# Kernel optimization log

Hardware: AMD Instinct MI355X
Metric: run time of the kernel (lower is better)

Reference implementation:

```python
import jax, jax.numpy as jnp
import numpy as np

B, T, D, H, C = 64, 1024, 128, 512, 2


def setup_inputs() -> dict:
    key = jax.random.key(0)
    ks = jax.random.split(key, 6)
    x = jax.random.normal(ks[0], (B, T, D), dtype=jnp.float32)
    labels = jax.random.randint(ks[1], (B, T), 0, C, dtype=jnp.int32)
    # Keras LSTMCell params: kernel [D,4H], recurrent_kernel [H,4H], bias [4H]
    Wx = jax.random.normal(ks[2], (D, 4 * H), dtype=jnp.float32) * (1.0 / np.sqrt(D))
    Wh = jax.random.normal(ks[3], (H, 4 * H), dtype=jnp.float32) * (1.0 / np.sqrt(H))
    b = jnp.zeros((4 * H,), dtype=jnp.float32).at[H:2 * H].set(1.0)  # unit forget bias
    Wo = jax.random.normal(ks[4], (H, C), dtype=jnp.float32) * (1.0 / np.sqrt(H))
    bo = jnp.zeros((C,), dtype=jnp.float32)
    return {"x": x, "labels": labels, "Wx": Wx, "Wh": Wh, "b": b, "Wo": Wo, "bo": bo}


def _lstm_logits(x, Wx, Wh, b, Wo, bo):
    # Precompute input contribution for all steps: [B,T,4H]
    xz = jnp.einsum('btd,dk->btk', x, Wx) + b

    def step(carry, z_t):
        h, c = carry
        z = z_t + h @ Wh                     # [B,4H]
        i, f, g, o = jnp.split(z, 4, axis=-1)  # keras gate order: i,f,c,o
        i = jax.nn.sigmoid(i)
        f = jax.nn.sigmoid(f)
        g = jnp.tanh(g)
        o = jax.nn.sigmoid(o)
        c = f * c + i * g
        h = o * jnp.tanh(c)
        return (h, c), h

    h0 = jnp.zeros((x.shape[0], Wh.shape[0]), dtype=x.dtype)
    (_, _), hs = jax.lax.scan(step, (h0, h0), jnp.swapaxes(xz, 0, 1))
    hs = jnp.swapaxes(hs, 0, 1)              # [B,T,H]
    return jnp.einsum('bth,hc->btc', hs, Wo) + bo  # [B,T,C]


def reference(x, labels, Wx, Wh, b, Wo, bo):
    logits = _lstm_logits(x, Wx, Wh, b, Wo, bo)
    logp = jax.nn.log_softmax(logits, axis=-1)
    prediction = jnp.exp(logp)               # softmax probs
    nll = -jnp.take_along_axis(logp, labels[..., None].astype(jnp.int32), axis=-1)[..., 0]
    cost = jnp.mean(nll)
    return prediction, cost
```

## Files before the change

kernel.cpp:

```cpp
#include <hip/hip_runtime.h>
#include <stdint.h>

#define TLEN 1024
#define BATCH 64
#define DIMX 128
#define HID 512

typedef __attribute__((ext_vector_type(8))) short short8;
typedef __attribute__((ext_vector_type(4))) float f32x4;
typedef __attribute__((ext_vector_type(4))) unsigned u32x4;

#define OFF_WT   0u
#define OFF_XBF  2621440u
#define OFF_HB   19398656u
#define OFF_ACC  19660800u
#define ZERO_LEN (262144u + 64u)

__device__ __forceinline__ unsigned short f2bf(float f) {
  unsigned u = __float_as_uint(f);
  u += 0x7fffu + ((u >> 16) & 1u);
  return (unsigned short)(u >> 16);
}
__device__ __forceinline__ float sigm(float x) { return 1.0f / (1.0f + __expf(-x)); }
__device__ __forceinline__ float tanh_fast(float x) {
  float a = fabsf(x);
  float e = __expf(2.0f * a);
  float t = 1.0f - 2.0f / (e + 1.0f);
  return copysignf(t, x);
}

__global__ void k_convx(const float4* __restrict__ x4, ushort4* __restrict__ o4) {
  int i = blockIdx.x * 256 + threadIdx.x;
  float4 v = x4[i];
  ushort4 o;
  o.x = f2bf(v.x); o.y = f2bf(v.y); o.z = f2bf(v.z); o.w = f2bf(v.w);
  o4[i] = o;
}

__global__ void k_tw(const float* __restrict__ Wx, const float* __restrict__ Wh,
                     unsigned short* __restrict__ Wt) {
  __shared__ float tile[32][65];
  int bk = blockIdx.x;
  int k0 = (bk / 64) * 64;
  int c0 = (bk % 64) * 32;
  int tid = threadIdx.x;
  const float* src = (k0 < 128) ? (Wx + (size_t)k0 * 2048)
                                : (Wh + (size_t)(k0 - 128) * 2048);
#pragma unroll
  for (int p = 0; p < 8; ++p) {
    int i = p * 256 + tid;
    int kk = i >> 5, cc = i & 31;
    tile[cc][kk] = src[(size_t)kk * 2048 + (c0 + cc)];
  }
  __syncthreads();
  int cc = tid >> 3, ch = tid & 7;
  unsigned short tmp[8];
#pragma unroll
  for (int j = 0; j < 8; ++j) tmp[j] = f2bf(tile[cc][ch * 8 + j]);
  uint4 o;
  o.x = (unsigned)tmp[0] | ((unsigned)tmp[1] << 16);
  o.y = (unsigned)tmp[2] | ((unsigned)tmp[3] << 16);
  o.z = (unsigned)tmp[4] | ((unsigned)tmp[5] << 16);
  o.w = (unsigned)tmp[6] | ((unsigned)tmp[7] << 16);
  *(uint4*)(Wt + (size_t)(c0 + cc) * 640 + k0 + ch * 8) = o;
}

__global__ __launch_bounds__(512, 1) void k_lstm(
    const unsigned short* __restrict__ xbf,
    const unsigned short* __restrict__ Wt,
    const float* __restrict__ bias,
    const float* __restrict__ Wo,
    unsigned* __restrict__ hb,
    float* __restrict__ out)
{
  __shared__ float red[2][4][4][8][32];
  __shared__ short8 xch[2][4][2][2][64];
  __shared__ unsigned xflag[2][4][2];

  const int tid  = threadIdx.x;
  const int w    = tid >> 6;
  const int kw   = w & 3;
  const int cg   = w >> 2;
  const int lane = tid & 63;
  const int q    = lane >> 4;
  const int m    = lane & 15;
  const int grp  = blockIdx.x & 7;
  const int hj   = blockIdx.x >> 3;
  const int g0   = grp * 8;

  if (tid < 16) xflag[tid >> 3][(tid >> 1) & 3][tid & 1] = 0;

  short8 Bf[5][4];
#pragma unroll
  for (int cc = 0; cc < 5; ++cc) {
#pragma unroll
    for (int j = 0; j < 4; ++j) {
      int gate = cg * 2 + (j >> 1);
      int col = gate * HID + hj * 32 + (j & 1) * 16 + m;
      int k = (cc == 0) ? (kw * 32 + q * 8)
                        : (128 + kw * 128 + (cc - 1) * 32 + q * 8);
      Bf[cc][j] = *(const short8*)(Wt + (size_t)col * 640 + k);
    }
  }

  const int col  = lane & 31;
  const int hcol = hj * 32 + col;
  float c_state = 0.0f;
  const float b_i = bias[0 * HID + hcol];
  const float b_f = bias[1 * HID + hcol];
  const float b_g = bias[2 * HID + hcol];
  const float b_o = bias[3 * HID + hcol];
  const float2 wo = ((const float2*)Wo)[hcol];

  const int ab = g0 + (m & 7);

  __syncthreads();

  short8 a0 = *(const short8*)(xbf + (size_t)ab * (TLEN * DIMX) + kw * 32 + q * 8);

#pragma unroll 1
  for (int t = 0; t < TLEN; ++t) {
    const unsigned* hin = hb + (size_t)(t & 1) * (BATCH * HID);
    const int buf = t & 1;

    const unsigned* pb = hin + (size_t)ab * HID + kw * 128 + cg * 64 + q * 8;
    u32x4 r0, r1, r2, r3;
    {
      const unsigned tg = (unsigned)t & 0xFFFFu;
      int guard = 0;
      for (;;) {
        asm volatile(
            "global_load_dwordx4 %0, %4, off sc0 sc1\n\t"
            "global_load_dwordx4 %1, %4, off offset:16 sc0 sc1\n\t"
            "global_load_dwordx4 %2, %4, off offset:128 sc0 sc1\n\t"
            "global_load_dwordx4 %3, %4, off offset:144 sc0 sc1\n\t"
            "s_waitcnt vmcnt(0)"
            : "=v"(r0), "=v"(r1), "=v"(r2), "=v"(r3)
            : "v"(pb)
            : "memory");
        unsigned d = (r0[0] ^ tg) | (r0[1] ^ tg) | (r0[2] ^ tg) | (r0[3] ^ tg);
        d |= (r1[0] ^ tg) | (r1[1] ^ tg) | (r1[2] ^ tg) | (r1[3] ^ tg);
        d |= (r2[0] ^ tg) | (r2[1] ^ tg) | (r2[2] ^ tg) | (r2[3] ^ tg);
        d |= (r3[0] ^ tg) | (r3[1] ^ tg) | (r3[2] ^ tg) | (r3[3] ^ tg);
        bool bad = (d & 0xFFFFu) != 0u;
        if (__ballot(bad) == 0ull || ++guard > (1 << 20)) break;
        __builtin_amdgcn_s_sleep(2);
      }
    }

    short8 f0, f1;
    {
      union { short8 s; unsigned u[4]; } pk;
      pk.u[0] = (r0[0] >> 16) | (r0[1] & 0xFFFF0000u);
      pk.u[1] = (r0[2] >> 16) | (r0[3] & 0xFFFF0000u);
      pk.u[2] = (r1[0] >> 16) | (r1[1] & 0xFFFF0000u);
      pk.u[3] = (r1[2] >> 16) | (r1[3] & 0xFFFF0000u);
      f0 = pk.s;
      pk.u[0] = (r2[0] >> 16) | (r2[1] & 0xFFFF0000u);
      pk.u[1] = (r2[2] >> 16) | (r2[3] & 0xFFFF0000u);
      pk.u[2] = (r3[0] >> 16) | (r3[1] & 0xFFFF0000u);
      pk.u[3] = (r3[2] >> 16) | (r3[3] & 0xFFFF0000u);
      f1 = pk.s;
    }

    xch[buf][kw][cg][0][lane] = f0;
    xch[buf][kw][cg][1][lane] = f1;
    __hip_atomic_store(&xflag[buf][kw][cg], (unsigned)(t + 1),
                       __ATOMIC_RELEASE, __HIP_MEMORY_SCOPE_WORKGROUP);
    {
      int guard = 0;
      while (__hip_atomic_load(&xflag[buf][kw][cg ^ 1], __ATOMIC_ACQUIRE,
                               __HIP_MEMORY_SCOPE_WORKGROUP) < (unsigned)(t + 1)) {
        if (++guard > (1 << 22)) break;
      }
    }
    short8 s0 = xch[buf][kw][cg ^ 1][0][lane];
    short8 s1 = xch[buf][kw][cg ^ 1][1][lane];

    short8 a1 = cg ? s0 : f0;
    short8 a2 = cg ? s1 : f1;
    short8 a3 = cg ? f0 : s0;
    short8 a4 = cg ? f1 : s1;

    f32x4 z0 = {0,0,0,0}, z1 = {0,0,0,0}, z2 = {0,0,0,0}, z3 = {0,0,0,0};
    z0 = __builtin_amdgcn_mfma_f32_16x16x32_bf16(a0, Bf[0][0], z0, 0, 0, 0);
    z1 = __builtin_amdgcn_mfma_f32_16x16x32_bf16(a0, Bf[0][1], z1, 0, 0, 0);
    z2 = __builtin_amdgcn_mfma_f32_16x16x32_bf16(a0, Bf[0][2], z2, 0, 0, 0);
    z3 = __builtin_amdgcn_mfma_f32_16x16x32_bf16(a0, Bf[0][3], z3, 0, 0, 0);
    z0 = __builtin_amdgcn_mfma_f32_16x16x32_bf16(a1, Bf[1][0], z0, 0, 0, 0);
    z1 = __builtin_amdgcn_mfma_f32_16x16x32_bf16(a1, Bf[1][1], z1, 0, 0, 0);
    z2 = __builtin_amdgcn_mfma_f32_16x16x32_bf16(a1, Bf[1][2], z2, 0, 0, 0);
    z3 = __builtin_amdgcn_mfma_f32_16x16x32_bf16(a1, Bf[1][3], z3, 0, 0, 0);
    z0 = __builtin_amdgcn_mfma_f32_16x16x32_bf16(a2, Bf[2][0], z0, 0, 0, 0);
    z1 = __builtin_amdgcn_mfma_f32_16x16x32_bf16(a2, Bf[2][1], z1, 0, 0, 0);
    z2 = __builtin_amdgcn_mfma_f32_16x16x32_bf16(a2, Bf[2][2], z2, 0, 0, 0);
    z3 = __builtin_amdgcn_mfma_f32_16x16x32_bf16(a2, Bf[2][3], z3, 0, 0, 0);
    z0 = __builtin_amdgcn_mfma_f32_16x16x32_bf16(a3, Bf[3][0], z0, 0, 0, 0);
    z1 = __builtin_amdgcn_mfma_f32_16x16x32_bf16(a3, Bf[3][1], z1, 0, 0, 0);
    z2 = __builtin_amdgcn_mfma_f32_16x16x32_bf16(a3, Bf[3][2], z2, 0, 0, 0);
    z3 = __builtin_amdgcn_mfma_f32_16x16x32_bf16(a3, Bf[3][3], z3, 0, 0, 0);
    z0 = __builtin_amdgcn_mfma_f32_16x16x32_bf16(a4, Bf[4][0], z0, 0, 0, 0);
    z1 = __builtin_amdgcn_mfma_f32_16x16x32_bf16(a4, Bf[4][1], z1, 0, 0, 0);
    z2 = __builtin_amdgcn_mfma_f32_16x16x32_bf16(a4, Bf[4][2], z2, 0, 0, 0);
    z3 = __builtin_amdgcn_mfma_f32_16x16x32_bf16(a4, Bf[4][3], z3, 0, 0, 0);

    {
      int tn = (t + 1 < TLEN) ? (t + 1) : t;
      a0 = *(const short8*)(xbf + ((size_t)ab * TLEN + tn) * DIMX +
                            kw * 32 + q * 8);
    }

    if (q < 2) {
#pragma unroll
      for (int r = 0; r < 4; ++r) {
        int rw = q * 4 + r;
        red[buf][kw][cg * 2 + 0][rw][0 * 16 + m] = z0[r];
        red[buf][kw][cg * 2 + 0][rw][1 * 16 + m] = z1[r];
        red[buf][kw][cg * 2 + 1][rw][0 * 16 + m] = z2[r];
        red[buf][kw][cg * 2 + 1][rw][1 * 16 + m] = z3[r];
      }
    }
    __syncthreads();

    if (lane < 32) {
      float zi = b_i + red[buf][0][0][w][col] + red[buf][1][0][w][col]
                     + red[buf][2][0][w][col] + red[buf][3][0][w][col];
      float zf = b_f + red[buf][0][1][w][col] + red[buf][1][1][w][col]
                     + red[buf][2][1][w][col] + red[buf][3][1][w][col];
      float zg = b_g + red[buf][0][2][w][col] + red[buf][1][2][w][col]
                     + red[buf][2][2][w][col] + red[buf][3][2][w][col];
      float zo = b_o + red[buf][0][3][w][col] + red[buf][1][3][w][col]
                     + red[buf][2][3][w][col] + red[buf][3][3][w][col];
      float ig = sigm(zi), fg = sigm(zf), gg = tanh_fast(zg), og = sigm(zo);
      c_state = fg * c_state + ig * gg;
      float hval = og * tanh_fast(c_state);

      unsigned hword = ((unsigned)f2bf(hval) << 16) | (unsigned)((t + 1) & 0xFFFF);
      int base = lane & ~3;
      unsigned w0 = __shfl(hword, base + 0);
      unsigned w1 = __shfl(hword, base + 1);
      unsigned w2 = __shfl(hword, base + 2);
      unsigned w3 = __shfl(hword, base + 3);
      if ((lane & 3) == 0) {
        u32x4 v4 = {w0, w1, w2, w3};
        unsigned* dst = hb + (size_t)((t + 1) & 1) * (BATCH * HID) +
                        (size_t)(g0 + w) * HID + hcol;
        asm volatile("global_store_dwordx4 %0, %1, off sc0 sc1"
                     :: "v"(dst), "v"(v4) : "memory");
      }

      float p0 = hval * wo.x, p1 = hval * wo.y;
      p0 += __shfl_xor(p0, 16); p1 += __shfl_xor(p1, 16);
      p0 += __shfl_xor(p0, 8);  p1 += __shfl_xor(p1, 8);
      p0 += __shfl_xor(p0, 4);  p1 += __shfl_xor(p1, 4);
      p0 += __shfl_xor(p0, 2);  p1 += __shfl_xor(p1, 2);
      p0 += __shfl_xor(p0, 1);  p1 += __shfl_xor(p1, 1);
      if (lane == 0) {
        float* po = out + ((size_t)(g0 + w) * TLEN + t) * 2;
        atomicAdd(po + 0, p0);
        atomicAdd(po + 1, p1);
      }
    }
  }
}

__global__ void k_out2(float* __restrict__ out, const float* __restrict__ bo,
                       const int* __restrict__ labels, float* __restrict__ acc) {
  __shared__ float sred[4];
  int i = blockIdx.x * 256 + threadIdx.x;
  float l0 = out[(size_t)i * 2 + 0] + bo[0];
  float l1 = out[(size_t)i * 2 + 1] + bo[1];
  float mx = fmaxf(l0, l1);
  float e0 = __expf(l0 - mx), e1 = __expf(l1 - mx);
  float s = e0 + e1, inv = 1.0f / s;
  out[(size_t)i * 2 + 0] = e0 * inv;
  out[(size_t)i * 2 + 1] = e1 * inv;
  int lab = labels[i];
  float nll = __logf(s) - ((lab ? l1 : l0) - mx);
#pragma unroll
  for (int off = 32; off >= 1; off >>= 1) nll += __shfl_xor(nll, off);
  if ((threadIdx.x & 63) == 0) sred[threadIdx.x >> 6] = nll;
  __syncthreads();
  if (threadIdx.x == 0)
    atomicAdd(acc, sred[0] + sred[1] + sred[2] + sred[3]);
}

__global__ void k_fin(const float* __restrict__ acc, float* __restrict__ out) {
  out[BATCH * TLEN * 2] = acc[0] * (1.0f / (float)(BATCH * TLEN));
}

extern "C" void kernel_launch(void* const* d_in, const int* in_sizes, int n_in,
                              void* d_out, int out_size, void* d_ws, size_t ws_size,
                              hipStream_t stream) {
  const float* x      = (const float*)d_in[0];
  const int*   labels = (const int*)d_in[1];
  const float* Wx     = (const float*)d_in[2];
  const float* Wh     = (const float*)d_in[3];
  const float* b      = (const float*)d_in[4];
  const float* Wo     = (const float*)d_in[5];
  const float* bo     = (const float*)d_in[6];
  float* out = (float*)d_out;
  char* ws = (char*)d_ws;

  unsigned short* Wt  = (unsigned short*)(ws + OFF_WT);
  unsigned short* xbf = (unsigned short*)(ws + OFF_XBF);
  unsigned*       hb  = (unsigned*)(ws + OFF_HB);
  float*          acc = (float*)(ws + OFF_ACC);

  hipMemsetAsync(ws + OFF_HB, 0, ZERO_LEN, stream);
  hipMemsetAsync(d_out, 0, (size_t)BATCH * TLEN * 2 * sizeof(float), stream);
  k_convx<<<8192, 256, 0, stream>>>((const float4*)x, (ushort4*)xbf);
  k_tw<<<640, 256, 0, stream>>>(Wx, Wh, Wt);
  k_lstm<<<128, 512, 0, stream>>>(xbf, Wt, b, Wo, hb, out);
  k_out2<<<256, 256, 0, stream>>>(out, bo, labels, acc);
  k_fin<<<1, 1, 0, stream>>>(acc, out);
}
```

Baseline: 3.113 ms.

## Halve LSTM block count by giving each block 64 hidden columns

```diff
diff --git a/kernel.cpp b/kernel.cpp
--- a/kernel.cpp
+++ b/kernel.cpp
@@ -65,7 +65,7 @@
   *(uint4*)(Wt + (size_t)(c0 + cc) * 640 + k0 + ch * 8) = o;
 }
 
-__global__ __launch_bounds__(512, 1) void k_lstm(
+__global__ __launch_bounds__(512, 2) void k_lstm(
     const unsigned short* __restrict__ xbf,
     const unsigned short* __restrict__ Wt,
     const float* __restrict__ bias,
@@ -73,7 +73,7 @@
     unsigned* __restrict__ hb,
     float* __restrict__ out)
 {
-  __shared__ float red[2][4][4][8][32];
+  __shared__ float red[2][4][4][8][64];
   __shared__ short8 xch[2][4][2][2][64];
   __shared__ unsigned xflag[2][4][2];
 
@@ -85,26 +85,25 @@
   const int q    = lane >> 4;
   const int m    = lane & 15;
   const int grp  = blockIdx.x & 7;
-  const int hj   = blockIdx.x >> 3;
+  const int hw   = blockIdx.x >> 3;
   const int g0   = grp * 8;
 
   if (tid < 16) xflag[tid >> 3][(tid >> 1) & 3][tid & 1] = 0;
 
-  short8 Bf[5][4];
-#pragma unroll
-  for (int cc = 0; cc < 5; ++cc) {
-#pragma unroll
-    for (int j = 0; j < 4; ++j) {
-      int gate = cg * 2 + (j >> 1);
-      int col = gate * HID + hj * 32 + (j & 1) * 16 + m;
-      int k = (cc == 0) ? (kw * 32 + q * 8)
-                        : (128 + kw * 128 + (cc - 1) * 32 + q * 8);
-      Bf[cc][j] = *(const short8*)(Wt + (size_t)col * 640 + k);
+  short8 Bf[5][8];
+#pragma unroll
+  for (int c = 0; c < 5; ++c) {
+#pragma unroll
+    for (int j = 0; j < 8; ++j) {
+      int gate = j >> 1;
+      int col = gate * HID + hw * 64 + cg * 32 + (j & 1) * 16 + m;
+      int k = (c == 0) ? (kw * 32 + q * 8)
+                       : (128 + kw * 128 + (c - 1) * 32 + q * 8);
+      Bf[c][j] = *(const short8*)(Wt + (size_t)col * 640 + k);
     }
   }
 
-  const int col  = lane & 31;
-  const int hcol = hj * 32 + col;
+  const int hcol = hw * 64 + lane;
   float c_state = 0.0f;
   const float b_i = bias[0 * HID + hcol];
   const float b_f = bias[1 * HID + hcol];
@@ -144,7 +143,6 @@
         d |= (r3[0] ^ tg) | (r3[1] ^ tg) | (r3[2] ^ tg) | (r3[3] ^ tg);
         bool bad = (d & 0xFFFFu) != 0u;
         if (__ballot(bad) == 0ull || ++guard > (1 << 20)) break;
-        __builtin_amdgcn_s_sleep(2);
       }
     }
 
@@ -182,27 +180,17 @@
     short8 a3 = cg ? f0 : s0;
     short8 a4 = cg ? f1 : s1;
 
-    f32x4 z0 = {0,0,0,0}, z1 = {0,0,0,0}, z2 = {0,0,0,0}, z3 = {0,0,0,0};
-    z0 = __builtin_amdgcn_mfma_f32_16x16x32_bf16(a0, Bf[0][0], z0, 0, 0, 0);
-    z1 = __builtin_amdgcn_mfma_f32_16x16x32_bf16(a0, Bf[0][1], z1, 0, 0, 0);
-    z2 = __builtin_amdgcn_mfma_f32_16x16x32_bf16(a0, Bf[0][2], z2, 0, 0, 0);
-    z3 = __builtin_amdgcn_mfma_f32_16x16x32_bf16(a0, Bf[0][3], z3, 0, 0, 0);
-    z0 = __builtin_amdgcn_mfma_f32_16x16x32_bf16(a1, Bf[1][0], z0, 0, 0, 0);
-    z1 = __builtin_amdgcn_mfma_f32_16x16x32_bf16(a1, Bf[1][1], z1, 0, 0, 0);
-    z2 = __builtin_amdgcn_mfma_f32_16x16x32_bf16(a1, Bf[1][2], z2, 0, 0, 0);
-    z3 = __builtin_amdgcn_mfma_f32_16x16x32_bf16(a1, Bf[1][3], z3, 0, 0, 0);
-    z0 = __builtin_amdgcn_mfma_f32_16x16x32_bf16(a2, Bf[2][0], z0, 0, 0, 0);
-    z1 = __builtin_amdgcn_mfma_f32_16x16x32_bf16(a2, Bf[2][1], z1, 0, 0, 0);
-    z2 = __builtin_amdgcn_mfma_f32_16x16x32_bf16(a2, Bf[2][2], z2, 0, 0, 0);
-    z3 = __builtin_amdgcn_mfma_f32_16x16x32_bf16(a2, Bf[2][3], z3, 0, 0, 0);
-    z0 = __builtin_amdgcn_mfma_f32_16x16x32_bf16(a3, Bf[3][0], z0, 0, 0, 0);
-    z1 = __builtin_amdgcn_mfma_f32_16x16x32_bf16(a3, Bf[3][1], z1, 0, 0, 0);
-    z2 = __builtin_amdgcn_mfma_f32_16x16x32_bf16(a3, Bf[3][2], z2, 0, 0, 0);
-    z3 = __builtin_amdgcn_mfma_f32_16x16x32_bf16(a3, Bf[3][3], z3, 0, 0, 0);
-    z0 = __builtin_amdgcn_mfma_f32_16x16x32_bf16(a4, Bf[4][0], z0, 0, 0, 0);
-    z1 = __builtin_amdgcn_mfma_f32_16x16x32_bf16(a4, Bf[4][1], z1, 0, 0, 0);
-    z2 = __builtin_amdgcn_mfma_f32_16x16x32_bf16(a4, Bf[4][2], z2, 0, 0, 0);
-    z3 = __builtin_amdgcn_mfma_f32_16x16x32_bf16(a4, Bf[4][3], z3, 0, 0, 0);
+    short8 A[5] = {a0, a1, a2, a3, a4};
+    f32x4 acc[8];
+#pragma unroll
+    for (int j = 0; j < 8; ++j) acc[j] = (f32x4){0.f, 0.f, 0.f, 0.f};
+#pragma unroll
+    for (int c = 0; c < 5; ++c) {
+#pragma unroll
+      for (int j = 0; j < 8; ++j)
+        acc[j] = __builtin_amdgcn_mfma_f32_16x16x32_bf16(A[c], Bf[c][j], acc[j],
+                                                         0, 0, 0);
+    }
 
     {
       int tn = (t + 1 < TLEN) ? (t + 1) : t;
@@ -212,25 +200,25 @@
 
     if (q < 2) {
 #pragma unroll
-      for (int r = 0; r < 4; ++r) {
-        int rw = q * 4 + r;
-        red[buf][kw][cg * 2 + 0][rw][0 * 16 + m] = z0[r];
-        red[buf][kw][cg * 2 + 0][rw][1 * 16 + m] = z1[r];
-        red[buf][kw][cg * 2 + 1][rw][0 * 16 + m] = z2[r];
-        red[buf][kw][cg * 2 + 1][rw][1 * 16 + m] = z3[r];
+      for (int j = 0; j < 8; ++j) {
+        int gate = j >> 1;
+        int lc = cg * 32 + (j & 1) * 16 + m;
+#pragma unroll
+        for (int r = 0; r < 4; ++r)
+          red[buf][kw][gate][q * 4 + r][lc] = acc[j][r];
       }
     }
     __syncthreads();
 
-    if (lane < 32) {
-      float zi = b_i + red[buf][0][0][w][col] + red[buf][1][0][w][col]
-                     + red[buf][2][0][w][col] + red[buf][3][0][w][col];
-      float zf = b_f + red[buf][0][1][w][col] + red[buf][1][1][w][col]
-                     + red[buf][2][1][w][col] + red[buf][3][1][w][col];
-      float zg = b_g + red[buf][0][2][w][col] + red[buf][1][2][w][col]
-                     + red[buf][2][2][w][col] + red[buf][3][2][w][col];
-      float zo = b_o + red[buf][0][3][w][col] + red[buf][1][3][w][col]
-                     + red[buf][2][3][w][col] + red[buf][3][3][w][col];
+    {
+      float zi = b_i + red[buf][0][0][w][lane] + red[buf][1][0][w][lane]
+                     + red[buf][2][0][w][lane] + red[buf][3][0][w][lane];
+      float zf = b_f + red[buf][0][1][w][lane] + red[buf][1][1][w][lane]
+                     + red[buf][2][1][w][lane] + red[buf][3][1][w][lane];
+      float zg = b_g + red[buf][0][2][w][lane] + red[buf][1][2][w][lane]
+                     + red[buf][2][2][w][lane] + red[buf][3][2][w][lane];
+      float zo = b_o + red[buf][0][3][w][lane] + red[buf][1][3][w][lane]
+                     + red[buf][2][3][w][lane] + red[buf][3][3][w][lane];
       float ig = sigm(zi), fg = sigm(zf), gg = tanh_fast(zg), og = sigm(zo);
       c_state = fg * c_state + ig * gg;
       float hval = og * tanh_fast(c_state);
@@ -244,12 +232,13 @@
       if ((lane & 3) == 0) {
         u32x4 v4 = {w0, w1, w2, w3};
         unsigned* dst = hb + (size_t)((t + 1) & 1) * (BATCH * HID) +
-                        (size_t)(g0 + w) * HID + hcol;
+                        (size_t)(g0 + w) * HID + hw * 64 + base;
         asm volatile("global_store_dwordx4 %0, %1, off sc0 sc1"
                      :: "v"(dst), "v"(v4) : "memory");
       }
 
       float p0 = hval * wo.x, p1 = hval * wo.y;
+      p0 += __shfl_xor(p0, 32); p1 += __shfl_xor(p1, 32);
       p0 += __shfl_xor(p0, 16); p1 += __shfl_xor(p1, 16);
       p0 += __shfl_xor(p0, 8);  p1 += __shfl_xor(p1, 8);
       p0 += __shfl_xor(p0, 4);  p1 += __shfl_xor(p1, 4);
@@ -311,7 +300,7 @@
   hipMemsetAsync(d_out, 0, (size_t)BATCH * TLEN * 2 * sizeof(float), stream);
   k_convx<<<8192, 256, 0, stream>>>((const float4*)x, (ushort4*)xbf);
   k_tw<<<640, 256, 0, stream>>>(Wx, Wh, Wt);
-  k_lstm<<<128, 512, 0, stream>>>(xbf, Wt, b, Wo, hb, out);
+  k_lstm<<<64, 512, 0, stream>>>(xbf, Wt, b, Wo, hb, out);
   k_out2<<<256, 256, 0, stream>>>(out, bo, labels, acc);
   k_fin<<<1, 1, 0, stream>>>(acc, out);
 }
```

Result: no change. 3.155 ms (+1.3%).
